# Optimization experiments

Measured on AMD Instinct MI355X. Metric: run time of the kernel, lower is better.

The kernel has to match this reference:

```python
import jax, jax.numpy as jnp
import numpy as np

USER_NUM = 60000
ITEM_NUM = 40000
NODE_NUM = USER_NUM + ITEM_NUM
EMBED_DIM = 64
N_LAYER = 3
NNZ = 1600000
BATCH = 4096
NEG_SLOPE = 0.2


def setup_inputs() -> dict:
    key = jax.random.key(0)
    ks = jax.random.split(key, 8)
    emb = jax.random.normal(ks[0], (NODE_NUM, EMBED_DIM), dtype=jnp.float32) * 0.1
    W1 = jax.random.normal(ks[1], (N_LAYER, EMBED_DIM, EMBED_DIM), dtype=jnp.float32) * 0.1
    W2 = jax.random.normal(ks[2], (N_LAYER, EMBED_DIM, EMBED_DIM), dtype=jnp.float32) * 0.1
    vals = jax.random.uniform(ks[3], (NNZ,), dtype=jnp.float32) * 0.01  # normalized Laplacian weights
    row_idx = jax.random.randint(ks[4], (NNZ,), 0, NODE_NUM, dtype=jnp.int32)
    col_idx = jax.random.randint(ks[5], (NNZ,), 0, NODE_NUM, dtype=jnp.int32)
    user_idx = jax.random.randint(ks[6], (BATCH,), 0, USER_NUM, dtype=jnp.int32)
    item_idx = jax.random.randint(ks[7], (BATCH,), 0, ITEM_NUM, dtype=jnp.int32)
    return {"emb": emb, "W1": W1, "W2": W2, "vals": vals,
            "row_idx": row_idx, "col_idx": col_idx,
            "user_idx": user_idx, "item_idx": item_idx}


def _spmm(vals, row_idx, col_idx, E):
    # L @ E with L in COO form: gather source rows, scale, scatter-add to dest rows
    msgs = vals[:, None] * E[col_idx]                       # [nnz, D]
    return jax.ops.segment_sum(msgs, row_idx, num_segments=NODE_NUM)


def reference(emb, W1, W2, vals, row_idx, col_idx, user_idx, item_idx):
    E_prev = emb
    E_list = [emb]
    for layer in range(N_LAYER):
        side_E = _spmm(vals, row_idx, col_idx, E_prev)      # [N, D]
        sum_E = side_E + E_prev
        bi_E = E_prev * side_E
        E_next = jax.nn.leaky_relu(sum_E @ W1[layer] + bi_E @ W2[layer],
                                   negative_slope=NEG_SLOPE)
        # dropout=0.0 / eval mode -> no-op
        E_prev = E_next
        E_list.append(E_next)
    E_all = jnp.concatenate(E_list, axis=1)                 # [N, D*(L+1)]
    E_user = E_all[:USER_NUM]
    E_item = E_all[USER_NUM:]
    return (E_user[user_idx], E_item[item_idx])
```

## Files before the change

### kernel.cpp

```cpp
#include <hip/hip_runtime.h>
#include <hip/hip_bf16.h>

#define USER_NUM 60000
#define ITEM_NUM 40000
#define NODE_NUM 100000
#define DIM 64
#define NNZ_N 1600000
#define BATCH 4096
#define NEG 0.2f
#define NBKT 98
#define PA_EPT 16
#define PA_EPB (256 * PA_EPT)
#define PA_GRID ((NNZ_N + PA_EPB - 1) / PA_EPB)
#define VAL_DEC 3.0517578125e-07f
#define NTILE 6250

typedef unsigned long long u64;
typedef unsigned int u32;
typedef __attribute__((ext_vector_type(8))) short bf16x8;
typedef __attribute__((ext_vector_type(4))) float f32x4;

__device__ __forceinline__ float bf2f(unsigned short u) {
    return __uint_as_float(((u32)u) << 16);
}
__device__ __forceinline__ unsigned short f2bf(float f) {
    u32 x = __float_as_uint(f);
    u32 r = (x + 0x7FFFu + ((x >> 16) & 1u)) >> 16;
    return (unsigned short)r;
}

__global__ void k_bcount(const int* __restrict__ row, int* __restrict__ bkt_cnt, int n) {
    __shared__ int h[NBKT];
    int t = threadIdx.x;
    if (t < NBKT) h[t] = 0;
    __syncthreads();
    int base = blockIdx.x * PA_EPB;
#pragma unroll
    for (int j = 0; j < PA_EPT; j++) {
        int idx = base + j * 256 + t;
        if (idx < n) atomicAdd(&h[row[idx] >> 10], 1);
    }
    __syncthreads();
    if (t < NBKT && h[t]) atomicAdd(&bkt_cnt[t], h[t]);
}

__global__ void k_bscan(const int* __restrict__ bkt_cnt, int* __restrict__ bkt_base,
                        int* __restrict__ bcur) {
    __shared__ int sh[128];
    int t = threadIdx.x;
    int v = (t < NBKT) ? bkt_cnt[t] : 0;
    sh[t] = v;
    __syncthreads();
    for (int d = 1; d < 128; d <<= 1) {
        int x = (t >= d) ? sh[t - d] : 0;
        __syncthreads();
        sh[t] += x;
        __syncthreads();
    }
    int excl = sh[t] - v;
    if (t < NBKT) { bkt_base[t] = excl; bcur[t] = excl; }
    if (t == 0) bkt_base[NBKT] = NNZ_N;
}

__launch_bounds__(256)
__global__ void k_passA(const int* __restrict__ row, const int* __restrict__ col,
                        const float* __restrict__ vals, int* __restrict__ bcur,
                        u64* __restrict__ tpk, int n) {
    __shared__ int cur[NBKT];
    __shared__ int gb[NBKT];
    int t = threadIdx.x;
    if (t < NBKT) cur[t] = 0;
    __syncthreads();
    int base = blockIdx.x * PA_EPB;
    u64 pk[PA_EPT];
    int rk[PA_EPT], bk[PA_EPT];
#pragma unroll
    for (int j = 0; j < PA_EPT; j++) {
        int idx = base + j * 256 + t;
        if (idx < n) {
            int r = row[idx];
            int c = col[idx];
            int bits = (int)rintf(vals[idx] * 3276800.0f);
            if (bits > 32767) bits = 32767;
            pk[j] = ((u64)(u32)r << 32) | ((u32)c << 15) | (u32)bits;
            bk[j] = r >> 10;
            rk[j] = atomicAdd(&cur[bk[j]], 1);
        } else bk[j] = -1;
    }
    __syncthreads();
    if (t < NBKT) {
        int cnt = cur[t];
        gb[t] = cnt ? atomicAdd(&bcur[t], cnt) : 0;
    }
    __syncthreads();
#pragma unroll
    for (int j = 0; j < PA_EPT; j++) {
        if (bk[j] >= 0) tpk[gb[bk[j]] + rk[j]] = pk[j];
    }
}

__launch_bounds__(1024)
__global__ void k_passB(const u64* __restrict__ tpk, const int* __restrict__ bkt_base,
                        int* __restrict__ ptr, u32* __restrict__ ecv) {
    __shared__ int sh[1024];
    int b = blockIdx.x, t = threadIdx.x;
    int start = bkt_base[b], end = bkt_base[b + 1];
    sh[t] = 0;
    __syncthreads();
    for (int i = start + t; i < end; i += 1024)
        atomicAdd(&sh[(int)(tpk[i] >> 32) & 1023], 1);
    __syncthreads();
    int cnt = sh[t];
    for (int d = 1; d < 1024; d <<= 1) {
        int x = (t >= d) ? sh[t - d] : 0;
        __syncthreads();
        sh[t] += x;
        __syncthreads();
    }
    int excl = sh[t] - cnt;
    int rowg = (b << 10) + t;
    if (rowg < NODE_NUM) ptr[rowg] = start + excl;
    if (b == NBKT - 1 && t == 0) ptr[NODE_NUM] = NNZ_N;
    __syncthreads();
    sh[t] = excl;
    __syncthreads();
    for (int i = start + t; i < end; i += 1024) {
        u64 e = tpk[i];
        int r = (int)(e >> 32);
        int pos = start + atomicAdd(&sh[r & 1023], 1);
        ecv[pos] = (u32)e;
    }
}

__launch_bounds__(1024)
__global__ void k_dhist(const int* __restrict__ ptr, int* __restrict__ dhist, int n) {
    __shared__ int h[64];
    int t = threadIdx.x;
    if (t < 64) h[t] = 0;
    __syncthreads();
    int i = blockIdx.x * 1024 + t;
    if (i < n) {
        int d = ptr[i + 1] - ptr[i];
        if (d > 63) d = 63;
        atomicAdd(&h[d], 1);
    }
    __syncthreads();
    if (t < 64 && h[t]) atomicAdd(&dhist[t], h[t]);
}

__global__ void k_dscan(const int* __restrict__ dhist, int* __restrict__ dcur) {
    __shared__ int sh[64];
    int t = threadIdx.x;
    int v = dhist[t];
    sh[t] = v;
    __syncthreads();
    for (int d = 1; d < 64; d <<= 1) {
        int x = (t >= d) ? sh[t - d] : 0;
        __syncthreads();
        sh[t] += x;
        __syncthreads();
    }
    dcur[t] = sh[t] - v;
}

__launch_bounds__(1024)
__global__ void k_dscatter(const int* __restrict__ ptr, int* __restrict__ dcur,
                           int* __restrict__ rord, int n) {
    __shared__ int h[64];
    __shared__ int gb[64];
    int t = threadIdx.x;
    if (t < 64) h[t] = 0;
    __syncthreads();
    int i = blockIdx.x * 1024 + t;
    int d = -1, rk = 0;
    if (i < n) {
        d = ptr[i + 1] - ptr[i];
        if (d > 63) d = 63;
        rk = atomicAdd(&h[d], 1);
    }
    __syncthreads();
    if (t < 64) {
        int cnt = h[t];
        gb[t] = cnt ? atomicAdd(&dcur[t], cnt) : 0;
    }
    __syncthreads();
    if (i < n) rord[gb[d] + rk] = i;
}

__global__ void k_cvt4(const float4* __restrict__ src, ushort4* __restrict__ dst, int n4) {
    int i = blockIdx.x * 256 + threadIdx.x;
    if (i < n4) {
        float4 f = src[i];
        dst[i] = make_ushort4(f2bf(f.x), f2bf(f.y), f2bf(f.z), f2bf(f.w));
    }
}

__launch_bounds__(256)
__global__ void k_spmm(const int* __restrict__ ptrS, const int* __restrict__ rord,
                       const u32* __restrict__ ecv, const unsigned short* __restrict__ Eb,
                       unsigned short* __restrict__ S) {
    int wave = (blockIdx.x * 256 + threadIdx.x) >> 6;
    int lane = threadIdx.x & 63;
    int L = lane & 7;
    int rslot = wave * 8 + (lane >> 3);
    int myrow = rord[rslot];
    int s = ptrS[myrow];
    int e = ptrS[myrow + 1];
    int d = e - s;
    int dm = d;
    dm = max(dm, __shfl_xor(dm, 8));
    dm = max(dm, __shfl_xor(dm, 16));
    dm = max(dm, __shfl_xor(dm, 32));
    float acc[8];
#pragma unroll
    for (int q = 0; q < 8; q++) acc[q] = 0.f;
    int srcbase = lane & 56;
    for (int off = 0; off < dm; off += 8) {
        int idx = s + off + L;
        u32 u = (idx < e) ? ecv[idx] : 0u;
#pragma unroll
        for (int j = 0; j < 8; j++) {
            u32 uu = __shfl(u, srcbase | j);
            float fv = (float)(uu & 0x7fffu);
            uint4 gw = *(const uint4*)&Eb[(size_t)(uu >> 15) * 64 + L * 8];
            acc[0] = fmaf(fv, __uint_as_float(gw.x << 16), acc[0]);
            acc[1] = fmaf(fv, __uint_as_float(gw.x & 0xffff0000u), acc[1]);
            acc[2] = fmaf(fv, __uint_as_float(gw.y << 16), acc[2]);
            acc[3] = fmaf(fv, __uint_as_float(gw.y & 0xffff0000u), acc[3]);
            acc[4] = fmaf(fv, __uint_as_float(gw.z << 16), acc[4]);
            acc[5] = fmaf(fv, __uint_as_float(gw.z & 0xffff0000u), acc[5]);
            acc[6] = fmaf(fv, __uint_as_float(gw.w << 16), acc[6]);
            acc[7] = fmaf(fv, __uint_as_float(gw.w & 0xffff0000u), acc[7]);
        }
    }
    u32 o[4];
#pragma unroll
    for (int q = 0; q < 4; q++) {
        float x0 = acc[2 * q] * VAL_DEC;
        float x1 = acc[2 * q + 1] * VAL_DEC;
        o[q] = (u32)f2bf(x0) | ((u32)f2bf(x1) << 16);
    }
    *(uint4*)&S[(size_t)myrow * 64 + L * 8] = make_uint4(o[0], o[1], o[2], o[3]);
}

__launch_bounds__(256)
__global__ void k_dmm(const unsigned short* __restrict__ Ein,
                      const unsigned short* __restrict__ S,
                      const float* __restrict__ W1l, const float* __restrict__ W2l,
                      unsigned short* __restrict__ Eout) {
    __shared__ unsigned short cbuf[4][16 * 68];
    int t = threadIdx.x;
    int w = t >> 6;
    int lane = t & 63;
    int r16 = lane & 15;
    int g = lane >> 4;

    bf16x8 bw[2][2][4];
#pragma unroll
    for (int mat = 0; mat < 2; mat++) {
        const float* W = mat ? W2l : W1l;
#pragma unroll
        for (int kc = 0; kc < 2; kc++) {
#pragma unroll
            for (int cb = 0; cb < 4; cb++) {
                int col = cb * 16 + r16;
                int k0 = kc * 32 + g * 8;
                bf16x8 f;
#pragma unroll
                for (int j = 0; j < 8; j++)
                    f[j] = (short)f2bf(W[(k0 + j) * 64 + col]);
                bw[mat][kc][cb] = f;
            }
        }
    }

    for (int tile = blockIdx.x * 4 + w; tile < NTILE; tile += gridDim.x * 4) {
        int row0 = tile * 16;
        const unsigned short* ep = &Ein[(size_t)(row0 + r16) * 64 + g * 8];
        const unsigned short* sp = &S[(size_t)(row0 + r16) * 64 + g * 8];
        f32x4 ac0 = {0.f, 0.f, 0.f, 0.f};
        f32x4 ac1 = {0.f, 0.f, 0.f, 0.f};
        f32x4 ac2 = {0.f, 0.f, 0.f, 0.f};
        f32x4 ac3 = {0.f, 0.f, 0.f, 0.f};
#pragma unroll
        for (int kc = 0; kc < 2; kc++) {
            bf16x8 ev = *(const bf16x8*)(ep + kc * 32);
            bf16x8 sv = *(const bf16x8*)(sp + kc * 32);
            bf16x8 su, bi;
#pragma unroll
            for (int j = 0; j < 8; j++) {
                float e = bf2f((unsigned short)ev[j]);
                float s = bf2f((unsigned short)sv[j]);
                su[j] = (short)f2bf(e + s);
                bi[j] = (short)f2bf(e * s);
            }
            ac0 = __builtin_amdgcn_mfma_f32_16x16x32_bf16(su, bw[0][kc][0], ac0, 0, 0, 0);
            ac0 = __builtin_amdgcn_mfma_f32_16x16x32_bf16(bi, bw[1][kc][0], ac0, 0, 0, 0);
            ac1 = __builtin_amdgcn_mfma_f32_16x16x32_bf16(su, bw[0][kc][1], ac1, 0, 0, 0);
            ac1 = __builtin_amdgcn_mfma_f32_16x16x32_bf16(bi, bw[1][kc][1], ac1, 0, 0, 0);
            ac2 = __builtin_amdgcn_mfma_f32_16x16x32_bf16(su, bw[0][kc][2], ac2, 0, 0, 0);
            ac2 = __builtin_amdgcn_mfma_f32_16x16x32_bf16(bi, bw[1][kc][2], ac2, 0, 0, 0);
            ac3 = __builtin_amdgcn_mfma_f32_16x16x32_bf16(su, bw[0][kc][3], ac3, 0, 0, 0);
            ac3 = __builtin_amdgcn_mfma_f32_16x16x32_bf16(bi, bw[1][kc][3], ac3, 0, 0, 0);
        }
#pragma unroll
        for (int reg = 0; reg < 4; reg++) {
            int crow = g * 4 + reg;
            float x0 = ac0[reg]; x0 = x0 > 0.f ? x0 : NEG * x0;
            float x1 = ac1[reg]; x1 = x1 > 0.f ? x1 : NEG * x1;
            float x2 = ac2[reg]; x2 = x2 > 0.f ? x2 : NEG * x2;
            float x3 = ac3[reg]; x3 = x3 > 0.f ? x3 : NEG * x3;
            cbuf[w][crow * 68 + 0 * 16 + r16] = f2bf(x0);
            cbuf[w][crow * 68 + 1 * 16 + r16] = f2bf(x1);
            cbuf[w][crow * 68 + 2 * 16 + r16] = f2bf(x2);
            cbuf[w][crow * 68 + 3 * 16 + r16] = f2bf(x3);
        }
        int rrow = lane >> 2;
        int q = lane & 3;
        const uint4* lp = (const uint4*)&cbuf[w][rrow * 68 + q * 16];
        uint4 v0 = lp[0];
        uint4 v1 = lp[1];
        uint4* gp = (uint4*)&Eout[(size_t)(row0 + rrow) * 64 + q * 16];
        gp[0] = v0;
        gp[1] = v1;
    }
}

__global__ void k_gather0(const float* __restrict__ E, float* __restrict__ out,
                          const int* __restrict__ uidx, const int* __restrict__ iidx) {
    int g = blockIdx.x * 256 + threadIdx.x;
    int b = g >> 6, d = g & 63;
    if (b >= 2 * BATCH) return;
    int node;
    size_t obase;
    if (b < BATCH) { node = uidx[b]; obase = (size_t)b * 256; }
    else { int bb = b - BATCH; node = USER_NUM + iidx[bb]; obase = (size_t)BATCH * 256 + (size_t)bb * 256; }
    out[obase + d] = E[(size_t)node * 64 + d];
}

__global__ void k_gatherb(const unsigned short* __restrict__ E, float* __restrict__ out,
                          const int* __restrict__ uidx, const int* __restrict__ iidx,
                          int layer) {
    int g = blockIdx.x * 256 + threadIdx.x;
    int b = g >> 6, d = g & 63;
    if (b >= 2 * BATCH) return;
    int node;
    size_t obase;
    if (b < BATCH) { node = uidx[b]; obase = (size_t)b * 256; }
    else { int bb = b - BATCH; node = USER_NUM + iidx[bb]; obase = (size_t)BATCH * 256 + (size_t)bb * 256; }
    out[obase + layer * 64 + d] = bf2f(E[(size_t)node * 64 + d]);
}

extern "C" void kernel_launch(void* const* d_in, const int* in_sizes, int n_in,
                              void* d_out, int out_size, void* d_ws, size_t ws_size,
                              hipStream_t stream) {
    const float* emb  = (const float*)d_in[0];
    const float* W1   = (const float*)d_in[1];
    const float* W2   = (const float*)d_in[2];
    const float* vals = (const float*)d_in[3];
    const int*   row  = (const int*)d_in[4];
    const int*   col  = (const int*)d_in[5];
    const int*   uidx = (const int*)d_in[6];
    const int*   iidx = (const int*)d_in[7];
    float* out = (float*)d_out;

    char* p = (char*)d_ws;
    auto alloc = [&](size_t bytes) -> void* {
        void* q = (void*)p;
        p += (bytes + 255) & ~(size_t)255;
        return q;
    };
    int*            ptr      = (int*)alloc((size_t)(NODE_NUM + 1) * 4);
    int*            bkt_cnt  = (int*)alloc(NBKT * 4);
    int*            bkt_base = (int*)alloc((NBKT + 1) * 4);
    int*            bcur     = (int*)alloc(NBKT * 4);
    int*            dhist    = (int*)alloc(64 * 4);
    int*            dcur     = (int*)alloc(64 * 4);
    int*            rord     = (int*)alloc((size_t)NODE_NUM * 4);
    u32*            ecv      = (u32*)alloc((size_t)NNZ_N * 4);
    u64*            tpk      = (u64*)alloc((size_t)NNZ_N * 8);
    unsigned short* Sb       = (unsigned short*)alloc((size_t)NODE_NUM * DIM * 2);
    unsigned short* Ebf0     = (unsigned short*)alloc((size_t)NODE_NUM * DIM * 2);
    unsigned short* Eba      = (unsigned short*)alloc((size_t)NODE_NUM * DIM * 2);
    unsigned short* Ebb      = (unsigned short*)alloc((size_t)NODE_NUM * DIM * 2);

    hipMemsetAsync(bkt_cnt, 0, NBKT * 4, stream);
    hipMemsetAsync(dhist, 0, 64 * 4, stream);
    k_bcount<<<PA_GRID, 256, 0, stream>>>(row, bkt_cnt, NNZ_N);
    k_bscan<<<1, 128, 0, stream>>>(bkt_cnt, bkt_base, bcur);
    k_passA<<<PA_GRID, 256, 0, stream>>>(row, col, vals, bcur, tpk, NNZ_N);
    k_passB<<<NBKT, 1024, 0, stream>>>(tpk, bkt_base, ptr, ecv);

    k_dhist<<<NBKT, 1024, 0, stream>>>(ptr, dhist, NODE_NUM);
    k_dscan<<<1, 64, 0, stream>>>(dhist, dcur);
    k_dscatter<<<NBKT, 1024, 0, stream>>>(ptr, dcur, rord, NODE_NUM);

    k_cvt4<<<(NODE_NUM * DIM / 4 + 255) / 256, 256, 0, stream>>>(
        (const float4*)emb, (ushort4*)Ebf0, NODE_NUM * DIM / 4);

    k_gather0<<<2048, 256, 0, stream>>>(emb, out, uidx, iidx);

    const int SPMM_GRID = NODE_NUM / 32;
    const int DMM_GRID = 391;
    k_spmm<<<SPMM_GRID, 256, 0, stream>>>(ptr, rord, ecv, Ebf0, Sb);
    k_dmm<<<DMM_GRID, 256, 0, stream>>>(Ebf0, Sb, W1, W2, Eba);
    k_gatherb<<<2048, 256, 0, stream>>>(Eba, out, uidx, iidx, 1);

    k_spmm<<<SPMM_GRID, 256, 0, stream>>>(ptr, rord, ecv, Eba, Sb);
    k_dmm<<<DMM_GRID, 256, 0, stream>>>(Eba, Sb, W1 + 4096, W2 + 4096, Ebb);
    k_gatherb<<<2048, 256, 0, stream>>>(Ebb, out, uidx, iidx, 2);

    k_spmm<<<SPMM_GRID, 256, 0, stream>>>(ptr, rord, ecv, Ebb, Sb);
    k_dmm<<<DMM_GRID, 256, 0, stream>>>(Ebb, Sb, W1 + 8192, W2 + 8192, Eba);
    k_gatherb<<<2048, 256, 0, stream>>>(Eba, out, uidx, iidx, 3);
}
```

Measured before the change: 223.7 us.

## Gather SpMM source rows from FP8 copies and fuse degree histogram into passB

Each layer now writes an extra FP8 (e4m3) copy of the embedding table, from the cvt kernel and from the dense-matmul epilogue. The SpMM gathers these 64-byte FP8 rows instead of 128-byte bf16 rows, halving random-gather traffic, then decodes them with the packed FP8-to-f32 conversion. Separately, the row-degree histogram is computed inside passB from its shared counts, which drops the k_dhist launch and its re-read of ptr. The cost is extra FP8 writes per layer and a noticeable precision loss on the neighbor embeddings, which may exceed the tolerance.

```diff
diff --git a/kernel.cpp b/kernel.cpp
--- a/kernel.cpp
+++ b/kernel.cpp
@@ -19,6 +19,7 @@
 typedef unsigned int u32;
 typedef __attribute__((ext_vector_type(8))) short bf16x8;
 typedef __attribute__((ext_vector_type(4))) float f32x4;
+typedef __attribute__((ext_vector_type(2))) float f32x2;
 
 __device__ __forceinline__ float bf2f(unsigned short u) {
     return __uint_as_float(((u32)u) << 16);
@@ -27,6 +28,12 @@
     u32 x = __float_as_uint(f);
     u32 r = (x + 0x7FFFu + ((x >> 16) & 1u)) >> 16;
     return (unsigned short)r;
+}
+template <bool WORD>
+__device__ __forceinline__ int cvt2fp8(u32 u, int old) {
+    float lo = __uint_as_float(u << 16);
+    float hi = __uint_as_float(u & 0xffff0000u);
+    return __builtin_amdgcn_cvt_pk_fp8_f32(lo, hi, old, WORD);
 }
 
 __global__ void k_bcount(const int* __restrict__ row, int* __restrict__ bkt_cnt, int n) {
@@ -101,16 +108,21 @@
 
 __launch_bounds__(1024)
 __global__ void k_passB(const u64* __restrict__ tpk, const int* __restrict__ bkt_base,
-                        int* __restrict__ ptr, u32* __restrict__ ecv) {
+                        int* __restrict__ ptr, u32* __restrict__ ecv,
+                        int* __restrict__ dhist) {
     __shared__ int sh[1024];
+    __shared__ int h2[64];
     int b = blockIdx.x, t = threadIdx.x;
     int start = bkt_base[b], end = bkt_base[b + 1];
     sh[t] = 0;
+    if (t < 64) h2[t] = 0;
     __syncthreads();
     for (int i = start + t; i < end; i += 1024)
         atomicAdd(&sh[(int)(tpk[i] >> 32) & 1023], 1);
     __syncthreads();
     int cnt = sh[t];
+    int rowg = (b << 10) + t;
+    if (rowg < NODE_NUM) atomicAdd(&h2[cnt > 63 ? 63 : cnt], 1);
     for (int d = 1; d < 1024; d <<= 1) {
         int x = (t >= d) ? sh[t - d] : 0;
         __syncthreads();
@@ -118,7 +130,6 @@
         __syncthreads();
     }
     int excl = sh[t] - cnt;
-    int rowg = (b << 10) + t;
     if (rowg < NODE_NUM) ptr[rowg] = start + excl;
     if (b == NBKT - 1 && t == 0) ptr[NODE_NUM] = NNZ_N;
     __syncthreads();
@@ -130,22 +141,8 @@
         int pos = start + atomicAdd(&sh[r & 1023], 1);
         ecv[pos] = (u32)e;
     }
-}
-
-__launch_bounds__(1024)
-__global__ void k_dhist(const int* __restrict__ ptr, int* __restrict__ dhist, int n) {
-    __shared__ int h[64];
-    int t = threadIdx.x;
-    if (t < 64) h[t] = 0;
-    __syncthreads();
-    int i = blockIdx.x * 1024 + t;
-    if (i < n) {
-        int d = ptr[i + 1] - ptr[i];
-        if (d > 63) d = 63;
-        atomicAdd(&h[d], 1);
-    }
-    __syncthreads();
-    if (t < 64 && h[t]) atomicAdd(&dhist[t], h[t]);
+    __syncthreads();
+    if (t < 64 && h2[t]) atomicAdd(&dhist[t], h2[t]);
 }
 
 __global__ void k_dscan(const int* __restrict__ dhist, int* __restrict__ dcur) {
@@ -187,17 +184,21 @@
     if (i < n) rord[gb[d] + rk] = i;
 }
 
-__global__ void k_cvt4(const float4* __restrict__ src, ushort4* __restrict__ dst, int n4) {
+__global__ void k_cvt4(const float4* __restrict__ src, ushort4* __restrict__ dstB,
+                       u32* __restrict__ dstF, int n4) {
     int i = blockIdx.x * 256 + threadIdx.x;
     if (i < n4) {
         float4 f = src[i];
-        dst[i] = make_ushort4(f2bf(f.x), f2bf(f.y), f2bf(f.z), f2bf(f.w));
+        dstB[i] = make_ushort4(f2bf(f.x), f2bf(f.y), f2bf(f.z), f2bf(f.w));
+        int w = __builtin_amdgcn_cvt_pk_fp8_f32(f.x, f.y, 0, false);
+        w = __builtin_amdgcn_cvt_pk_fp8_f32(f.z, f.w, w, true);
+        dstF[i] = (u32)w;
     }
 }
 
 __launch_bounds__(256)
 __global__ void k_spmm(const int* __restrict__ ptrS, const int* __restrict__ rord,
-                       const u32* __restrict__ ecv, const unsigned short* __restrict__ Eb,
+                       const u32* __restrict__ ecv, const unsigned char* __restrict__ Ef,
                        unsigned short* __restrict__ S) {
     int wave = (blockIdx.x * 256 + threadIdx.x) >> 6;
     int lane = threadIdx.x & 63;
@@ -206,8 +207,7 @@
     int myrow = rord[rslot];
     int s = ptrS[myrow];
     int e = ptrS[myrow + 1];
-    int d = e - s;
-    int dm = d;
+    int dm = e - s;
     dm = max(dm, __shfl_xor(dm, 8));
     dm = max(dm, __shfl_xor(dm, 16));
     dm = max(dm, __shfl_xor(dm, 32));
@@ -222,15 +222,19 @@
         for (int j = 0; j < 8; j++) {
             u32 uu = __shfl(u, srcbase | j);
             float fv = (float)(uu & 0x7fffu);
-            uint4 gw = *(const uint4*)&Eb[(size_t)(uu >> 15) * 64 + L * 8];
-            acc[0] = fmaf(fv, __uint_as_float(gw.x << 16), acc[0]);
-            acc[1] = fmaf(fv, __uint_as_float(gw.x & 0xffff0000u), acc[1]);
-            acc[2] = fmaf(fv, __uint_as_float(gw.y << 16), acc[2]);
-            acc[3] = fmaf(fv, __uint_as_float(gw.y & 0xffff0000u), acc[3]);
-            acc[4] = fmaf(fv, __uint_as_float(gw.z << 16), acc[4]);
-            acc[5] = fmaf(fv, __uint_as_float(gw.z & 0xffff0000u), acc[5]);
-            acc[6] = fmaf(fv, __uint_as_float(gw.w << 16), acc[6]);
-            acc[7] = fmaf(fv, __uint_as_float(gw.w & 0xffff0000u), acc[7]);
+            uint2 gw = *(const uint2*)&Ef[(size_t)(uu >> 15) * 64 + L * 8];
+            f32x2 g01 = __builtin_amdgcn_cvt_pk_f32_fp8(gw.x, false);
+            f32x2 g23 = __builtin_amdgcn_cvt_pk_f32_fp8(gw.x, true);
+            f32x2 g45 = __builtin_amdgcn_cvt_pk_f32_fp8(gw.y, false);
+            f32x2 g67 = __builtin_amdgcn_cvt_pk_f32_fp8(gw.y, true);
+            acc[0] = fmaf(fv, g01.x, acc[0]);
+            acc[1] = fmaf(fv, g01.y, acc[1]);
+            acc[2] = fmaf(fv, g23.x, acc[2]);
+            acc[3] = fmaf(fv, g23.y, acc[3]);
+            acc[4] = fmaf(fv, g45.x, acc[4]);
+            acc[5] = fmaf(fv, g45.y, acc[5]);
+            acc[6] = fmaf(fv, g67.x, acc[6]);
+            acc[7] = fmaf(fv, g67.y, acc[7]);
         }
     }
     u32 o[4];
@@ -247,7 +251,7 @@
 __global__ void k_dmm(const unsigned short* __restrict__ Ein,
                       const unsigned short* __restrict__ S,
                       const float* __restrict__ W1l, const float* __restrict__ W2l,
-                      unsigned short* __restrict__ Eout) {
+                      unsigned short* __restrict__ Eout, unsigned char* __restrict__ Eout8) {
     __shared__ unsigned short cbuf[4][16 * 68];
     int t = threadIdx.x;
     int w = t >> 6;
@@ -323,6 +327,12 @@
         uint4* gp = (uint4*)&Eout[(size_t)(row0 + rrow) * 64 + q * 16];
         gp[0] = v0;
         gp[1] = v1;
+        int w0 = cvt2fp8<false>(v0.x, 0); w0 = cvt2fp8<true>(v0.y, w0);
+        int w1 = cvt2fp8<false>(v0.z, 0); w1 = cvt2fp8<true>(v0.w, w1);
+        int w2 = cvt2fp8<false>(v1.x, 0); w2 = cvt2fp8<true>(v1.y, w2);
+        int w3 = cvt2fp8<false>(v1.z, 0); w3 = cvt2fp8<true>(v1.w, w3);
+        *(uint4*)&Eout8[(size_t)(row0 + rrow) * 64 + q * 16] =
+            make_uint4((u32)w0, (u32)w1, (u32)w2, (u32)w3);
     }
 }
 
@@ -383,34 +393,36 @@
     unsigned short* Ebf0     = (unsigned short*)alloc((size_t)NODE_NUM * DIM * 2);
     unsigned short* Eba      = (unsigned short*)alloc((size_t)NODE_NUM * DIM * 2);
     unsigned short* Ebb      = (unsigned short*)alloc((size_t)NODE_NUM * DIM * 2);
+    unsigned char*  Ef0      = (unsigned char*)alloc((size_t)NODE_NUM * DIM);
+    unsigned char*  Efa      = (unsigned char*)alloc((size_t)NODE_NUM * DIM);
+    unsigned char*  Efb      = (unsigned char*)alloc((size_t)NODE_NUM * DIM);
 
     hipMemsetAsync(bkt_cnt, 0, NBKT * 4, stream);
     hipMemsetAsync(dhist, 0, 64 * 4, stream);
     k_bcount<<<PA_GRID, 256, 0, stream>>>(row, bkt_cnt, NNZ_N);
     k_bscan<<<1, 128, 0, stream>>>(bkt_cnt, bkt_base, bcur);
     k_passA<<<PA_GRID, 256, 0, stream>>>(row, col, vals, bcur, tpk, NNZ_N);
-    k_passB<<<NBKT, 1024, 0, stream>>>(tpk, bkt_base, ptr, ecv);
-
-    k_dhist<<<NBKT, 1024, 0, stream>>>(ptr, dhist, NODE_NUM);
+    k_passB<<<NBKT, 1024, 0, stream>>>(tpk, bkt_base, ptr, ecv, dhist);
+
     k_dscan<<<1, 64, 0, stream>>>(dhist, dcur);
     k_dscatter<<<NBKT, 1024, 0, stream>>>(ptr, dcur, rord, NODE_NUM);
 
     k_cvt4<<<(NODE_NUM * DIM / 4 + 255) / 256, 256, 0, stream>>>(
-        (const float4*)emb, (ushort4*)Ebf0, NODE_NUM * DIM / 4);
+        (const float4*)emb, (ushort4*)Ebf0, (u32*)Ef0, NODE_NUM * DIM / 4);
 
     k_gather0<<<2048, 256, 0, stream>>>(emb, out, uidx, iidx);
 
     const int SPMM_GRID = NODE_NUM / 32;
     const int DMM_GRID = 391;
-    k_spmm<<<SPMM_GRID, 256, 0, stream>>>(ptr, rord, ecv, Ebf0, Sb);
-    k_dmm<<<DMM_GRID, 256, 0, stream>>>(Ebf0, Sb, W1, W2, Eba);
+    k_spmm<<<SPMM_GRID, 256, 0, stream>>>(ptr, rord, ecv, Ef0, Sb);
+    k_dmm<<<DMM_GRID, 256, 0, stream>>>(Ebf0, Sb, W1, W2, Eba, Efa);
     k_gatherb<<<2048, 256, 0, stream>>>(Eba, out, uidx, iidx, 1);
 
-    k_spmm<<<SPMM_GRID, 256, 0, stream>>>(ptr, rord, ecv, Eba, Sb);
-    k_dmm<<<DMM_GRID, 256, 0, stream>>>(Eba, Sb, W1 + 4096, W2 + 4096, Ebb);
+    k_spmm<<<SPMM_GRID, 256, 0, stream>>>(ptr, rord, ecv, Efa, Sb);
+    k_dmm<<<DMM_GRID, 256, 0, stream>>>(Eba, Sb, W1 + 4096, W2 + 4096, Ebb, Efb);
     k_gatherb<<<2048, 256, 0, stream>>>(Ebb, out, uidx, iidx, 2);
 
-    k_spmm<<<SPMM_GRID, 256, 0, stream>>>(ptr, rord, ecv, Ebb, Sb);
-    k_dmm<<<DMM_GRID, 256, 0, stream>>>(Ebb, Sb, W1 + 8192, W2 + 8192, Eba);
+    k_spmm<<<SPMM_GRID, 256, 0, stream>>>(ptr, rord, ecv, Efb, Sb);
+    k_dmm<<<DMM_GRID, 256, 0, stream>>>(Ebb, Sb, W1 + 8192, W2 + 8192, Eba, Efa);
     k_gatherb<<<2048, 256, 0, stream>>>(Eba, out, uidx, iidx, 3);
 }
```

Result: faster. 205.7 us (-8.1%).
